# Kernel optimization log

Measured on AMD Instinct MI355X. Metric: run time of the kernel, lower is better.

Reference implementation:

```python
import jax, jax.numpy as jnp
import numpy as np

EXP_BITS = 5
SIG_BITS = 10


def fp_quantize_ste(x, exp_bits=EXP_BITS, sig_bits=SIG_BITS):
    """Simulate a low-precision float format (round-to-nearest, subnormals on),
    with a straight-through estimator for gradients."""
    ebias = 2 ** (exp_bits - 1) - 1
    emin = 1 - ebias                      # min normal exponent; below -> subnormal
    emax = ebias
    xmax = (2.0 - 2.0 ** (-sig_bits)) * (2.0 ** emax)

    ax = jnp.abs(x)
    # exponent of each value; guard log2(0)
    e = jnp.floor(jnp.log2(jnp.where(ax > 0, ax, 1.0)))
    # clamping e below emin quantizes subnormals on the fixed 2^(emin-sig_bits) grid;
    # clamping above emax is handled by the final saturation to +-xmax
    e = jnp.clip(e, emin, emax)
    scale = jnp.exp2(sig_bits - e)        # quantization step = 2^(e - sig_bits)
    q = jnp.round(x * scale) / scale      # round-to-nearest (rmode=1)
    q = jnp.clip(q, -xmax, xmax)
    q = jnp.where(ax > 0, q, x)           # preserve exact zeros (and signed zero)
    # straight-through estimator: forward = q, backward = identity
    return x + jax.lax.stop_gradient(q - x)


def setup_inputs() -> dict:
    key = jax.random.key(0)
    k1, k2, k3 = jax.random.split(key, 3)
    N, D_IN, D_OUT = 8192, 4096, 4096
    x = jax.random.normal(k1, (N, D_IN), dtype=jnp.float32)
    weight = jax.random.normal(k2, (D_OUT, D_IN), dtype=jnp.float32) * (D_IN ** -0.5)
    bias = jax.random.normal(k3, (D_OUT,), dtype=jnp.float32) * 0.01
    return {"x": x, "weight": weight, "bias": bias}


def reference(x, weight, bias):
    xq = fp_quantize_ste(x)               # act_quant
    wq = fp_quantize_ste(weight)          # weight_quant
    bq = fp_quantize_ste(bias)            # bias quantized with weight_quant
    # F.linear: x @ W^T + b
    return jnp.einsum('ni,oi->no', xq, wq) + bq
```

## Files before the change

kernel.cpp:

```cpp
#include <hip/hip_runtime.h>
#include <hip/hip_fp16.h>
#include <cstdint>
#include <cstddef>

#define GLOBAL_AS __attribute__((address_space(1)))
#define LDS_AS    __attribute__((address_space(3)))

typedef __attribute__((ext_vector_type(8)))  _Float16 f16x8;
typedef __attribute__((ext_vector_type(16))) float    f32x16;

__device__ __forceinline__ void gload_lds16(const void* g, void* l) {
    __builtin_amdgcn_global_load_lds((const GLOBAL_AS void*)g,
                                     (LDS_AS void*)l, 16, 0, 0);
}

__device__ __forceinline__ __half qcvt(float x) {
    x = fminf(fmaxf(x, -65504.f), 65504.f);
    return __float2half(x);
}

__global__ void quant_xw_f32_to_f16(const float* __restrict__ xin, int x4,
                                    const float* __restrict__ win, int w4,
                                    __half* __restrict__ xout,
                                    __half* __restrict__ wout) {
    const int stride = gridDim.x * blockDim.x;
    const int tot = x4 + w4;
    for (int i = blockIdx.x * blockDim.x + threadIdx.x; i < tot; i += stride) {
        const bool isx = (i < x4);
        const int  j   = isx ? i : i - x4;
        const float4 f = reinterpret_cast<const float4*>(isx ? xin : win)[j];
        union { __half h[4]; uint2 u; } p;
        p.h[0] = qcvt(f.x);
        p.h[1] = qcvt(f.y);
        p.h[2] = qcvt(f.z);
        p.h[3] = qcvt(f.w);
        reinterpret_cast<uint2*>(isx ? xout : wout)[j] = p.u;
    }
}

__global__ __launch_bounds__(512, 2) void gemm_f16_32x32(
    const __half* __restrict__ A, const __half* __restrict__ B,
    const float* __restrict__ bias, float* __restrict__ C,
    int M, int N, int K)
{
    __shared__ __align__(16) __half lds[2][2][2][8192];

    const int tid  = threadIdx.x;
    const int lane = tid & 63;
    const int wid  = tid >> 6;
    const int wr   = wid >> 2;
    const int wc   = wid & 3;
    const int lr   = lane & 31;
    const int hi   = lane >> 5;

    const int nwg = gridDim.x;
    const int qq = nwg >> 3, rr = nwg & 7;
    const int xcd = blockIdx.x & 7, idx = blockIdx.x >> 3;
    const int wgid = (xcd < rr ? xcd * (qq + 1)
                               : rr * (qq + 1) + (xcd - rr) * qq) + idx;
    const int nbn = N >> 8;
    const int tile_m = (wgid / nbn) << 8;
    const int tile_n = (wgid % nbn) << 8;

    const int wbyte = (lane * 16) ^ (((lane >> 5) & 1) << 5);
    const int srow  = ((wid >> 1) << 4) + (wbyte >> 6);
    const int scb   = ((wid & 1) << 6) + (wbyte & 63);
    const char* gA0 = (const char*)A + (size_t)(tile_m + srow) * K * 2 + scb;
    const char* gB0 = (const char*)B + (size_t)(tile_n + srow) * K * 2 + scb;
    const size_t rstep = (size_t)64  * K * 2;
    const size_t hstep = (size_t)128 * K * 2;
    const int ldst = tid * 16;

    const uint32_t laneE = (uint32_t)((lr >> 4) * 2048 + (lr & 15) * 64
                                      + hi * 16 + (((lr >> 3) & 1) << 5));
    const uint32_t lds0 = (uint32_t)(size_t)(LDS_AS const char*)&lds[0][0][0][0];
    const uint32_t aE0 = lds0 + (uint32_t)(wr * 8192) + laneE;
    const uint32_t aO0 = aE0 ^ 32u;
    const uint32_t aE1 = aE0 + 65536u;
    const uint32_t aO1 = aE1 ^ 32u;
    const uint32_t bE0 = lds0 + 32768u + (uint32_t)(wc * 4096) + laneE;
    const uint32_t bO0 = bE0 ^ 32u;
    const uint32_t bE1 = bE0 + 65536u;
    const uint32_t bO1 = bE1 ^ 32u;

    f32x16 acc[2][2][2];
#pragma unroll
    for (int qa = 0; qa < 2; ++qa)
#pragma unroll
        for (int qb = 0; qb < 2; ++qb)
#pragma unroll
            for (int mm = 0; mm < 2; ++mm)
#pragma unroll
                for (int e = 0; e < 16; ++e)
                    acc[qa][qb][mm][e] = 0.f;

    f16x8 af[2][4];
    f16x8 bfP[4];
    f16x8 bfQ[4];

#define STAGE_A(bufi, h, kt) do {                                          \
        char* l_ = (char*)(&lds[bufi][0][h][0]) + ldst;                    \
        const char* g_ = gA0 + (size_t)(kt) * 128 + ((h) ? hstep : 0);     \
        gload_lds16(g_, l_);                                               \
        gload_lds16(g_ + rstep, l_ + 8192);                                \
    } while (0)

#define STAGE_B(bufi, h, kt) do {                                          \
        char* l_ = (char*)(&lds[bufi][1][h][0]) + ldst;                    \
        const char* g_ = gB0 + (size_t)(kt) * 128 + ((h) ? hstep : 0);     \
        gload_lds16(g_, l_);                                               \
        gload_lds16(g_ + rstep, l_ + 8192);                                \
    } while (0)

#define DSR(dst, base, OFF)                                                \
    asm volatile("ds_read_b128 %0, %1 offset:%c2"                          \
                 : "=v"(dst) : "v"(base), "i"(OFF))

#define LDGA(E, O, Q) do {                                                 \
        DSR(af[0][0], E, (Q)*16384 + 0);                                   \
        DSR(af[0][1], O, (Q)*16384 + 0);                                   \
        DSR(af[0][2], E, (Q)*16384 + 1024);                                \
        DSR(af[0][3], O, (Q)*16384 + 1024);                                \
        DSR(af[1][0], E, (Q)*16384 + 4096);                                \
        DSR(af[1][1], O, (Q)*16384 + 4096);                                \
        DSR(af[1][2], E, (Q)*16384 + 5120);                                \
        DSR(af[1][3], O, (Q)*16384 + 5120);                                \
    } while (0)

#define LDGB(dst, E, O, HB) do {                                           \
        DSR(dst[0], E, (HB)*16384 + 0);                                    \
        DSR(dst[1], O, (HB)*16384 + 0);                                    \
        DSR(dst[2], E, (HB)*16384 + 1024);                                 \
        DSR(dst[3], O, (HB)*16384 + 1024);                                 \
    } while (0)

#define MFMA32(A8, B8, ACC)                                                \
    ACC = __builtin_amdgcn_mfma_f32_32x32x16_f16(A8, B8, ACC, 0, 0, 0)

#define MMA4(QA, QB, MM, BF) do {                                          \
        __builtin_amdgcn_s_setprio(1);                                     \
        MFMA32(af[MM][0], BF[0], acc[QA][QB][MM]);                         \
        MFMA32(af[MM][1], BF[1], acc[QA][QB][MM]);                         \
        MFMA32(af[MM][2], BF[2], acc[QA][QB][MM]);                         \
        MFMA32(af[MM][3], BF[3], acc[QA][QB][MM]);                         \
        __builtin_amdgcn_s_setprio(0);                                     \
    } while (0)

#define MMA_KK2(QA, QB, K0, K1, BF) do {                                   \
        __builtin_amdgcn_s_setprio(1);                                     \
        MFMA32(af[0][K0], BF[K0], acc[QA][QB][0]);                         \
        MFMA32(af[1][K0], BF[K0], acc[QA][QB][1]);                         \
        MFMA32(af[0][K1], BF[K1], acc[QA][QB][0]);                         \
        MFMA32(af[1][K1], BF[K1], acc[QA][QB][1]);                         \
        __builtin_amdgcn_s_setprio(0);                                     \
    } while (0)

#define WAITL(NLIT)                                                        \
    asm volatile("s_waitcnt lgkmcnt(" NLIT ")");                           \
    __builtin_amdgcn_sched_barrier(0)

#define BARS()                                                             \
    __builtin_amdgcn_s_barrier();                                          \
    __builtin_amdgcn_sched_barrier(0)

#define TILE_FULL(AEc, AOc, BEc, BOc, BEn, BOn, CURB, NXTB, kt, SU, SV)    \
                       \
    LDGA(AEc, AOc, 0); STAGE_B(NXTB, 0, (kt) + 1);                         \
    WAITL("4"); MMA4(0, 0, 0, SU);                                         \
    WAITL("0"); MMA4(0, 0, 1, SU);                                         \
    BARS();                                                                \
                     \
    LDGB(SV, BEc, BOc, 1); STAGE_A(CURB, 0, (kt) + 2);                     \
    WAITL("2"); MMA_KK2(0, 1, 0, 1, SV);                                   \
    WAITL("0"); MMA_KK2(0, 1, 2, 3, SV);                                   \
    BARS();                                                                \
                          \
    LDGA(AEc, AOc, 1); STAGE_B(CURB, 1, (kt) + 2);                         \
    WAITL("4"); MMA4(1, 1, 0, SV);                                         \
    WAITL("0"); MMA4(1, 1, 1, SV);                                         \
    BARS();                                                                \
    \
    STAGE_A(CURB, 1, (kt) + 2);                                            \
    asm volatile("s_waitcnt vmcnt(6)");                                    \
    BARS();                                                                \
    LDGB(SV, BEn, BOn, 0);                                                 \
    __builtin_amdgcn_sched_barrier(0);                                     \
    MMA4(1, 0, 0, SU); MMA4(1, 0, 1, SU);                                  \
    BARS();

    STAGE_A(0, 0, 0); STAGE_B(0, 0, 0); STAGE_B(0, 1, 0); STAGE_A(0, 1, 0);
    STAGE_A(1, 0, 1); STAGE_B(1, 1, 1); STAGE_A(1, 1, 1);
    asm volatile("s_waitcnt vmcnt(6)");
    BARS();
    LDGB(bfP, bE0, bO0, 0);
    __builtin_amdgcn_sched_barrier(0);

    const int nt = K >> 6;
    for (int kt = 0; kt + 3 < nt; kt += 2) {
        TILE_FULL(aE0, aO0, bE0, bO0, bE1, bO1, 0, 1, kt,     bfP, bfQ);
        TILE_FULL(aE1, aO1, bE1, bO1, bE0, bO0, 1, 0, kt + 1, bfQ, bfP);
    }

    LDGA(aE0, aO0, 0); STAGE_B(1, 0, nt - 1);
    WAITL("4"); MMA4(0, 0, 0, bfP);
    WAITL("0"); MMA4(0, 0, 1, bfP);
    BARS();
    LDGB(bfQ, bE0, bO0, 1);
    WAITL("2"); MMA_KK2(0, 1, 0, 1, bfQ);
    WAITL("0"); MMA_KK2(0, 1, 2, 3, bfQ);
    BARS();
    LDGA(aE0, aO0, 1);
    WAITL("4"); MMA4(1, 1, 0, bfQ);
    WAITL("0"); MMA4(1, 1, 1, bfQ);
    BARS();
    asm volatile("s_waitcnt vmcnt(0)");
    BARS();
    LDGB(bfQ, bE1, bO1, 0);
    __builtin_amdgcn_sched_barrier(0);
    MMA4(1, 0, 0, bfP); MMA4(1, 0, 1, bfP);
    BARS();

    LDGA(aE1, aO1, 0);
    WAITL("4"); MMA4(0, 0, 0, bfQ);
    WAITL("0"); MMA4(0, 0, 1, bfQ);
    BARS();
    LDGB(bfP, bE1, bO1, 1);
    WAITL("2"); MMA_KK2(0, 1, 0, 1, bfP);
    WAITL("0"); MMA_KK2(0, 1, 2, 3, bfP);
    BARS();
    LDGA(aE1, aO1, 1);
    WAITL("4"); MMA4(1, 1, 0, bfP);
    WAITL("0"); MMA4(1, 1, 1, bfP);
    BARS();
    MMA4(1, 0, 0, bfQ); MMA4(1, 0, 1, bfQ);

    float bv[2];
#pragma unroll
    for (int qb = 0; qb < 2; ++qb)
        bv[qb] = __half2float(qcvt(bias[tile_n + qb * 128 + wc * 32 + lr]));

#pragma unroll
    for (int qa = 0; qa < 2; ++qa)
#pragma unroll
        for (int qb = 0; qb < 2; ++qb)
#pragma unroll
            for (int mm = 0; mm < 2; ++mm) {
                const int rowb = tile_m + qa * 128 + wr * 64 + mm * 32 + 4 * hi;
                const int col  = tile_n + qb * 128 + wc * 32 + lr;
#pragma unroll
                for (int g = 0; g < 4; ++g)
#pragma unroll
                    for (int s = 0; s < 4; ++s)
                        C[(size_t)(rowb + g * 8 + s) * N + col] =
                            acc[qa][qb][mm][g * 4 + s] + bv[qb];
            }

#undef STAGE_A
#undef STAGE_B
#undef DSR
#undef LDGA
#undef LDGB
#undef MFMA32
#undef MMA4
#undef MMA_KK2
#undef WAITL
#undef BARS
#undef TILE_FULL
}

__global__ void qat_gemm_naive(const float* __restrict__ A,
                               const float* __restrict__ B,
                               const float* __restrict__ bias,
                               float* __restrict__ C, int M, int N, int K) {
    const int col = blockIdx.x * blockDim.x + threadIdx.x;
    const int row = blockIdx.y;
    if (col >= N || row >= M) return;
    float s = 0.f;
    for (int k = 0; k < K; ++k) {
        float a = __half2float(qcvt(A[(size_t)row * K + k]));
        float b = __half2float(qcvt(B[(size_t)col * K + k]));
        s += a * b;
    }
    C[(size_t)row * N + col] = s + __half2float(qcvt(bias[col]));
}

extern "C" void kernel_launch(void* const* d_in, const int* in_sizes, int n_in,
                              void* d_out, int out_size, void* d_ws,
                              size_t ws_size, hipStream_t stream) {
    const float* x = (const float*)d_in[0];
    const float* w = (const float*)d_in[1];
    const float* b = (const float*)d_in[2];
    float* out = (float*)d_out;

    const int xn = in_sizes[0];
    const int wn = in_sizes[1];
    const int N  = in_sizes[2];
    const int K  = wn / N;
    const int M  = xn / K;

    const size_t need = (size_t)(xn + wn) * sizeof(__half);
    const bool ok = (M % 256 == 0) && (N % 256 == 0) &&
                    (K % 128 == 0) && (K >= 256);

    if (ws_size >= need && ok) {
        __half* xq = (__half*)d_ws;
        __half* wq = xq + xn;

        const int x4 = xn / 4, w4 = wn / 4;
        int blk = ((x4 + w4) + 255) / 256; if (blk > 2048) blk = 2048;
        quant_xw_f32_to_f16<<<blk, 256, 0, stream>>>(x, x4, w, w4, xq, wq);

        dim3 grid((M / 256) * (N / 256));
        gemm_f16_32x32<<<grid, 512, 0, stream>>>(xq, wq, b, out, M, N, K);
    } else {
        dim3 grid((N + 255) / 256, M);
        qat_gemm_naive<<<grid, 256, 0, stream>>>(x, w, b, out, M, N, K);
    }
}
```

Measured before the change: 306.8 us.

## Stage GEMM tiles into LDS in MFMA fragment order for linear reads

Global-to-LDS staging now places each lane's 16-byte chunk at the position its MFMA fragment expects. LDS reads become plain base + lane*16 with constant offsets, replacing the XOR-swizzled even/odd address pairs. This is meant to remove bank conflicts and address arithmetic on the LDS read side. The trade-off is that each wave's global loads now cover 32 rows at 32-byte granularity instead of longer contiguous row segments, which may hurt coalescing. Several sched_barrier fences were also dropped, leaving more instruction ordering to the compiler.

```diff
diff --git a/kernel.cpp b/kernel.cpp
--- a/kernel.cpp
+++ b/kernel.cpp
@@ -38,7 +38,7 @@
     }
 }
 
-__global__ __launch_bounds__(512, 2) void gemm_f16_32x32(
+__global__ __launch_bounds__(512, 2) void gemm_f16_fragorder(
     const __half* __restrict__ A, const __half* __restrict__ B,
     const float* __restrict__ bias, float* __restrict__ C,
     int M, int N, int K)
@@ -62,26 +62,19 @@
     const int tile_m = (wgid / nbn) << 8;
     const int tile_n = (wgid % nbn) << 8;
 
-    const int wbyte = (lane * 16) ^ (((lane >> 5) & 1) << 5);
-    const int srow  = ((wid >> 1) << 4) + (wbyte >> 6);
-    const int scb   = ((wid & 1) << 6) + (wbyte & 63);
+    const int srow = ((wid >> 2) << 5) + lr;
+    const int scb  = ((wid & 3) << 5) + (hi << 4);
     const char* gA0 = (const char*)A + (size_t)(tile_m + srow) * K * 2 + scb;
     const char* gB0 = (const char*)B + (size_t)(tile_n + srow) * K * 2 + scb;
     const size_t rstep = (size_t)64  * K * 2;
     const size_t hstep = (size_t)128 * K * 2;
     const int ldst = tid * 16;
 
-    const uint32_t laneE = (uint32_t)((lr >> 4) * 2048 + (lr & 15) * 64
-                                      + hi * 16 + (((lr >> 3) & 1) << 5));
     const uint32_t lds0 = (uint32_t)(size_t)(LDS_AS const char*)&lds[0][0][0][0];
-    const uint32_t aE0 = lds0 + (uint32_t)(wr * 8192) + laneE;
-    const uint32_t aO0 = aE0 ^ 32u;
-    const uint32_t aE1 = aE0 + 65536u;
-    const uint32_t aO1 = aE1 ^ 32u;
-    const uint32_t bE0 = lds0 + 32768u + (uint32_t)(wc * 4096) + laneE;
-    const uint32_t bO0 = bE0 ^ 32u;
-    const uint32_t bE1 = bE0 + 65536u;
-    const uint32_t bO1 = bE1 ^ 32u;
+    const uint32_t baseA0 = lds0 + (uint32_t)(wr * 8192 + lane * 16);
+    const uint32_t baseA1 = baseA0 + 65536u;
+    const uint32_t baseB0 = lds0 + 32768u + (uint32_t)(wc * 4096 + lane * 16);
+    const uint32_t baseB1 = baseB0 + 65536u;
 
     f32x16 acc[2][2][2];
 #pragma unroll
@@ -116,28 +109,28 @@
     asm volatile("ds_read_b128 %0, %1 offset:%c2"                          \
                  : "=v"(dst) : "v"(base), "i"(OFF))
 
-#define LDGA(E, O, Q) do {                                                 \
-        DSR(af[0][0], E, (Q)*16384 + 0);                                   \
-        DSR(af[0][1], O, (Q)*16384 + 0);                                   \
-        DSR(af[0][2], E, (Q)*16384 + 1024);                                \
-        DSR(af[0][3], O, (Q)*16384 + 1024);                                \
-        DSR(af[1][0], E, (Q)*16384 + 4096);                                \
-        DSR(af[1][1], O, (Q)*16384 + 4096);                                \
-        DSR(af[1][2], E, (Q)*16384 + 5120);                                \
-        DSR(af[1][3], O, (Q)*16384 + 5120);                                \
-    } while (0)
-
-#define LDGB(dst, E, O, HB) do {                                           \
-        DSR(dst[0], E, (HB)*16384 + 0);                                    \
-        DSR(dst[1], O, (HB)*16384 + 0);                                    \
-        DSR(dst[2], E, (HB)*16384 + 1024);                                 \
-        DSR(dst[3], O, (HB)*16384 + 1024);                                 \
+#define LDGA(BASE, H) do {                                                 \
+        DSR(af[0][0], BASE, (H)*16384 + 0);                                \
+        DSR(af[0][1], BASE, (H)*16384 + 1024);                             \
+        DSR(af[0][2], BASE, (H)*16384 + 2048);                             \
+        DSR(af[0][3], BASE, (H)*16384 + 3072);                             \
+        DSR(af[1][0], BASE, (H)*16384 + 4096);                             \
+        DSR(af[1][1], BASE, (H)*16384 + 5120);                             \
+        DSR(af[1][2], BASE, (H)*16384 + 6144);                             \
+        DSR(af[1][3], BASE, (H)*16384 + 7168);                             \
+    } while (0)
+
+#define LDGB(dst, BASE, H) do {                                            \
+        DSR(dst[0], BASE, (H)*16384 + 0);                                  \
+        DSR(dst[1], BASE, (H)*16384 + 1024);                               \
+        DSR(dst[2], BASE, (H)*16384 + 2048);                               \
+        DSR(dst[3], BASE, (H)*16384 + 3072);                               \
     } while (0)
 
 #define MFMA32(A8, B8, ACC)                                                \
     ACC = __builtin_amdgcn_mfma_f32_32x32x16_f16(A8, B8, ACC, 0, 0, 0)
 
-#define MMA4(QA, QB, MM, BF) do {                                          \
+#define MMA_MM(QA, QB, MM, BF) do {                                        \
         __builtin_amdgcn_s_setprio(1);                                     \
         MFMA32(af[MM][0], BF[0], acc[QA][QB][MM]);                         \
         MFMA32(af[MM][1], BF[1], acc[QA][QB][MM]);                         \
@@ -146,7 +139,7 @@
         __builtin_amdgcn_s_setprio(0);                                     \
     } while (0)
 
-#define MMA_KK2(QA, QB, K0, K1, BF) do {                                   \
+#define MMA_KK(QA, QB, K0, K1, BF) do {                                    \
         __builtin_amdgcn_s_setprio(1);                                     \
         MFMA32(af[0][K0], BF[K0], acc[QA][QB][0]);                         \
         MFMA32(af[1][K0], BF[K0], acc[QA][QB][1]);                         \
@@ -160,79 +153,75 @@
     __builtin_amdgcn_sched_barrier(0)
 
 #define BARS()                                                             \
-    __builtin_amdgcn_s_barrier();                                          \
-    __builtin_amdgcn_sched_barrier(0)
-
-#define TILE_FULL(AEc, AOc, BEc, BOc, BEn, BOn, CURB, NXTB, kt, SU, SV)    \
+    __builtin_amdgcn_s_barrier()
+
+#define TILE_FULL(ABASE, BBASE, BBASEn, CURB, NXTB, kt, SU, SV)            \
                        \
-    LDGA(AEc, AOc, 0); STAGE_B(NXTB, 0, (kt) + 1);                         \
-    WAITL("4"); MMA4(0, 0, 0, SU);                                         \
-    WAITL("0"); MMA4(0, 0, 1, SU);                                         \
+    LDGA(ABASE, 0); STAGE_B(NXTB, 0, (kt) + 1);                            \
+    WAITL("4"); MMA_MM(0, 0, 0, SU);                                       \
+    WAITL("0"); MMA_MM(0, 0, 1, SU);                                       \
     BARS();                                                                \
                      \
-    LDGB(SV, BEc, BOc, 1); STAGE_A(CURB, 0, (kt) + 2);                     \
-    WAITL("2"); MMA_KK2(0, 1, 0, 1, SV);                                   \
-    WAITL("0"); MMA_KK2(0, 1, 2, 3, SV);                                   \
+    LDGB(SV, BBASE, 1); STAGE_A(CURB, 0, (kt) + 2);                        \
+    WAITL("2"); MMA_KK(0, 1, 0, 1, SV);                                    \
+    WAITL("0"); MMA_KK(0, 1, 2, 3, SV);                                    \
     BARS();                                                                \
                           \
-    LDGA(AEc, AOc, 1); STAGE_B(CURB, 1, (kt) + 2);                         \
-    WAITL("4"); MMA4(1, 1, 0, SV);                                         \
-    WAITL("0"); MMA4(1, 1, 1, SV);                                         \
+    LDGA(ABASE, 1); STAGE_B(CURB, 1, (kt) + 2);                            \
+    WAITL("4"); MMA_MM(1, 1, 0, SV);                                       \
+    WAITL("0"); MMA_MM(1, 1, 1, SV);                                       \
     BARS();                                                                \
     \
     STAGE_A(CURB, 1, (kt) + 2);                                            \
     asm volatile("s_waitcnt vmcnt(6)");                                    \
     BARS();                                                                \
-    LDGB(SV, BEn, BOn, 0);                                                 \
-    __builtin_amdgcn_sched_barrier(0);                                     \
-    MMA4(1, 0, 0, SU); MMA4(1, 0, 1, SU);                                  \
+    LDGB(SV, BBASEn, 0);                                                   \
+    MMA_MM(1, 0, 0, SU); MMA_MM(1, 0, 1, SU);                              \
     BARS();
 
     STAGE_A(0, 0, 0); STAGE_B(0, 0, 0); STAGE_B(0, 1, 0); STAGE_A(0, 1, 0);
     STAGE_A(1, 0, 1); STAGE_B(1, 1, 1); STAGE_A(1, 1, 1);
     asm volatile("s_waitcnt vmcnt(6)");
     BARS();
-    LDGB(bfP, bE0, bO0, 0);
-    __builtin_amdgcn_sched_barrier(0);
+    LDGB(bfP, baseB0, 0);
 
     const int nt = K >> 6;
     for (int kt = 0; kt + 3 < nt; kt += 2) {
-        TILE_FULL(aE0, aO0, bE0, bO0, bE1, bO1, 0, 1, kt,     bfP, bfQ);
-        TILE_FULL(aE1, aO1, bE1, bO1, bE0, bO0, 1, 0, kt + 1, bfQ, bfP);
+        TILE_FULL(baseA0, baseB0, baseB1, 0, 1, kt,     bfP, bfQ);
+        TILE_FULL(baseA1, baseB1, baseB0, 1, 0, kt + 1, bfQ, bfP);
     }
 
-    LDGA(aE0, aO0, 0); STAGE_B(1, 0, nt - 1);
-    WAITL("4"); MMA4(0, 0, 0, bfP);
-    WAITL("0"); MMA4(0, 0, 1, bfP);
-    BARS();
-    LDGB(bfQ, bE0, bO0, 1);
-    WAITL("2"); MMA_KK2(0, 1, 0, 1, bfQ);
-    WAITL("0"); MMA_KK2(0, 1, 2, 3, bfQ);
-    BARS();
-    LDGA(aE0, aO0, 1);
-    WAITL("4"); MMA4(1, 1, 0, bfQ);
-    WAITL("0"); MMA4(1, 1, 1, bfQ);
+    LDGA(baseA0, 0); STAGE_B(1, 0, nt - 1);
+    WAITL("4"); MMA_MM(0, 0, 0, bfP);
+    WAITL("0"); MMA_MM(0, 0, 1, bfP);
+    BARS();
+    LDGB(bfQ, baseB0, 1);
+    WAITL("2"); MMA_KK(0, 1, 0, 1, bfQ);
+    WAITL("0"); MMA_KK(0, 1, 2, 3, bfQ);
+    BARS();
+    LDGA(baseA0, 1);
+    WAITL("4"); MMA_MM(1, 1, 0, bfQ);
+    WAITL("0"); MMA_MM(1, 1, 1, bfQ);
     BARS();
     asm volatile("s_waitcnt vmcnt(0)");
     BARS();
-    LDGB(bfQ, bE1, bO1, 0);
-    __builtin_amdgcn_sched_barrier(0);
-    MMA4(1, 0, 0, bfP); MMA4(1, 0, 1, bfP);
-    BARS();
-
-    LDGA(aE1, aO1, 0);
-    WAITL("4"); MMA4(0, 0, 0, bfQ);
-    WAITL("0"); MMA4(0, 0, 1, bfQ);
-    BARS();
-    LDGB(bfP, bE1, bO1, 1);
-    WAITL("2"); MMA_KK2(0, 1, 0, 1, bfP);
-    WAITL("0"); MMA_KK2(0, 1, 2, 3, bfP);
-    BARS();
-    LDGA(aE1, aO1, 1);
-    WAITL("4"); MMA4(1, 1, 0, bfP);
-    WAITL("0"); MMA4(1, 1, 1, bfP);
-    BARS();
-    MMA4(1, 0, 0, bfQ); MMA4(1, 0, 1, bfQ);
+    LDGB(bfQ, baseB1, 0);
+    MMA_MM(1, 0, 0, bfP); MMA_MM(1, 0, 1, bfP);
+    BARS();
+
+    LDGA(baseA1, 0);
+    WAITL("4"); MMA_MM(0, 0, 0, bfQ);
+    WAITL("0"); MMA_MM(0, 0, 1, bfQ);
+    BARS();
+    LDGB(bfP, baseB1, 1);
+    WAITL("2"); MMA_KK(0, 1, 0, 1, bfP);
+    WAITL("0"); MMA_KK(0, 1, 2, 3, bfP);
+    BARS();
+    LDGA(baseA1, 1);
+    WAITL("4"); MMA_MM(1, 1, 0, bfP);
+    WAITL("0"); MMA_MM(1, 1, 1, bfP);
+    BARS();
+    MMA_MM(1, 0, 0, bfQ); MMA_MM(1, 0, 1, bfQ);
 
     float bv[2];
 #pragma unroll
@@ -261,8 +250,8 @@
 #undef LDGA
 #undef LDGB
 #undef MFMA32
-#undef MMA4
-#undef MMA_KK2
+#undef MMA_MM
+#undef MMA_KK
 #undef WAITL
 #undef BARS
 #undef TILE_FULL
@@ -311,7 +300,7 @@
         quant_xw_f32_to_f16<<<blk, 256, 0, stream>>>(x, x4, w, w4, xq, wq);
 
         dim3 grid((M / 256) * (N / 256));
-        gemm_f16_32x32<<<grid, 512, 0, stream>>>(xq, wq, b, out, M, N, K);
+        gemm_f16_fragorder<<<grid, 512, 0, stream>>>(xq, wq, b, out, M, N, K);
     } else {
         dim3 grid((N + 255) / 256, M);
         qat_gemm_naive<<<grid, 256, 0, stream>>>(x, w, b, out, M, N, K);
```

Result: slower. 337.7 us (+10.1%).
